# Kernel optimization log

Measured on AMD Instinct MI355X. Metric: run time of the kernel, lower is better.

Reference implementation:

```python
import jax, jax.numpy as jnp
import numpy as np

NUM_HEADS = 12

def get_rel_pos(q_size, k_size, rel_pos):
    # q_size == k_size here; relative index = i - j + (k_size - 1)
    idx = jnp.arange(q_size)[:, None] - jnp.arange(k_size)[None, :] + (k_size - 1)
    return rel_pos[idx]  # (q_size, k_size, head_dim)


def setup_inputs() -> dict:
    key = jax.random.key(0)
    ks = jax.random.split(key, 7)
    B, H, W, C = 1, 64, 64, 768
    return {
        "x": jax.random.normal(ks[0], (B, H, W, C), jnp.float32),
        "w_qkv": jax.random.normal(ks[1], (C, 3 * C), jnp.float32) * 0.02,
        "b_qkv": jnp.zeros((3 * C,), jnp.float32),
        "w_o": jax.random.normal(ks[2], (C, C), jnp.float32) * 0.02,
        "b_o": jnp.zeros((C,), jnp.float32),
        "rel_pos_h": jax.random.normal(ks[3], (2 * H - 1, C // NUM_HEADS), jnp.float32) * 0.02,
        "rel_pos_w": jax.random.normal(ks[4], (2 * W - 1, C // NUM_HEADS), jnp.float32) * 0.02,
    }


def reference(x, w_qkv, b_qkv, w_o, b_o, rel_pos_h, rel_pos_w):
    B, H, W, C = x.shape
    NH = NUM_HEADS
    HD = C // NH
    scale = HD ** -0.5  # 0.125

    qkv = x @ w_qkv + b_qkv                                   # (B,H,W,3C)
    qkv = qkv.reshape(B, H * W, 3, NH, HD)
    qkv = jnp.transpose(qkv, (2, 0, 3, 1, 4)).reshape(3, B * NH, H * W, HD)
    q, k, v = qkv[0], qkv[1], qkv[2]                          # (B*NH, HW, HD)

    Rh = get_rel_pos(H, H, rel_pos_h)                         # (H,H,HD)
    Rw = get_rel_pos(W, W, rel_pos_w)                         # (W,W,HD)
    qr = q.reshape(B * NH, H, W, HD)
    rel_h = jnp.einsum('bhwc,hkc->bhwk', qr, Rh)              # (B*NH,H,W,H)
    rel_w = jnp.einsum('bhwc,wkc->bhwk', qr, Rw)              # (B*NH,H,W,W)

    attn = jnp.einsum('bmd,bnd->bmn', q, k) * scale           # (B*NH,HW,HW)
    attn = attn.reshape(B * NH, H, W, H, W)
    attn = attn + rel_h[:, :, :, :, None] + rel_w[:, :, :, None, :]
    attn = attn.reshape(B * NH, H * W, H * W)

    p = jax.nn.softmax(attn, axis=-1)
    o = jnp.einsum('bmn,bnd->bmd', p, v)                      # (B*NH,HW,HD)
    o = o.reshape(B, NH, H * W, HD)
    o = jnp.transpose(o, (0, 2, 1, 3)).reshape(B, H, W, C)    # heads concat in channel dim
    return o @ w_o + b_o
```

## Files before the change

### kernel.cpp

```cpp
#include <hip/hip_runtime.h>

#define DEVI __device__ __forceinline__
typedef unsigned short u16;
typedef unsigned int u32;
typedef __attribute__((ext_vector_type(4))) float f4v;
typedef __attribute__((ext_vector_type(8))) short bf8v;
typedef __attribute__((ext_vector_type(4))) u32  u32x4;
typedef __attribute__((ext_vector_type(2))) u32  u32x2;
typedef __attribute__((ext_vector_type(4))) u16  u16x4;

#define AS1 __attribute__((address_space(1)))
#define AS3 __attribute__((address_space(3)))

DEVI u16 f2bf(float x){ union{float f;u32 u;} c{x}; u32 r=(c.u+0x7FFFu+((c.u>>16)&1u))>>16; return (u16)r; }
DEVI float bf2f(u16 b){ union{u32 u;float f;} c{(u32)b<<16}; return c.f; }
DEVI f4v mfma32(bf8v a, bf8v b, f4v c){ return __builtin_amdgcn_mfma_f32_16x16x32_bf16(a,b,c,0,0,0); }
DEVI unsigned lds_off(const void* p){ return (unsigned)(unsigned long)(AS3 const void*)p; }
DEVI void glds16(const void* g, void* l){
  __builtin_amdgcn_global_load_lds((AS1 void*)g, (AS3 void*)l, 16, 0, 0);
}

static constexpr int NH = 12, HW = 4096, D = 64, C = 768;
static constexpr float LOG2E = 1.44269504f;

__global__ void qa_convx(const float* __restrict__ x, u16* __restrict__ xb, int n4){
  int i = blockIdx.x*256 + threadIdx.x;
  if(i >= n4) return;
  f4v v = ((const f4v*)x)[i];
  u16x4 o; for(int j=0;j<4;j++) o[j] = f2bf(v[j]);
  ((u16x4*)xb)[i] = o;
}

__global__ void qa_transp(const float* __restrict__ in, u16* __restrict__ out, int R, int Cc){
  __shared__ float tl[32][33];
  int t = threadIdx.x;
  int r0 = blockIdx.y*32, c0 = blockIdx.x*32;
  int tr = t>>3, tc = (t&7)*4;
  f4v v = *(const f4v*)&in[(r0+tr)*Cc + c0 + tc];
  for(int j=0;j<4;j++) tl[tr][tc+j] = v[j];
  __syncthreads();
  int oc = t>>3, orr = (t&7)*4;
  u16x4 o; for(int j=0;j<4;j++) o[j] = f2bf(tl[orr+j][oc]);
  *(u16x4*)&out[(c0+oc)*R + r0 + orr] = o;
}

__global__ __launch_bounds__(256,2) void qa_gemm_qkv(
    const u16* __restrict__ A, const u16* __restrict__ Bt, const float* __restrict__ bias,
    u16* __restrict__ qb, u16* __restrict__ kb, u16* __restrict__ vb){
  __shared__ u16 Al[128*32], Bl[128*32];
  const int t = threadIdx.x, lane = t&63, w = t>>6, c16 = lane&15, h4 = lane>>4;
  const int m0 = blockIdx.y*128, n0 = blockIdx.x*128;
  const int wr = w>>1, wc = w&1;
  f4v acc[4][4] = {};
  for(int k0 = 0; k0 < 768; k0 += 32){
    __syncthreads();
    for(int i=0;i<2;i++){
      int off = i*4096 + w*1024 + lane*16;
      int row = off>>6, kk = (off&63)>>1;
      glds16(A  + (size_t)(m0+row)*768 + k0 + kk, (u16*)Al + i*2048 + w*512);
      glds16(Bt + (size_t)(n0+row)*768 + k0 + kk, (u16*)Bl + i*2048 + w*512);
    }
    __syncthreads();
    bf8v a[4], b[4];
    for(int mt=0;mt<4;mt++) a[mt] = *(const bf8v*)&Al[(wr*64+mt*16+c16)*32 + h4*8];
    for(int nt=0;nt<4;nt++) b[nt] = *(const bf8v*)&Bl[(wc*64+nt*16+c16)*32 + h4*8];
    for(int mt=0;mt<4;mt++) for(int nt=0;nt<4;nt++) acc[mt][nt] = mfma32(a[mt], b[nt], acc[mt][nt]);
  }
  for(int nt=0;nt<4;nt++){
    int col = n0 + wc*64 + nt*16 + c16;
    float bv = bias[col];
    int which = col/768, head = (col>>6)%12, d = col&63;
    u16* dst = which==0 ? qb : (which==1 ? kb : vb);
    float sc = (which==1) ? 0.125f*LOG2E : 1.0f;
    for(int mt=0;mt<4;mt++) for(int r=0;r<4;r++){
      int row = m0 + wr*64 + mt*16 + 4*h4 + r;
      dst[((size_t)(head<<12)+row)*64 + d] = f2bf((acc[mt][nt][r] + bv)*sc);
    }
  }
}

__global__ __launch_bounds__(256) void qa_rel(
    const u16* __restrict__ qbuf, const float* __restrict__ rph, const float* __restrict__ rpw,
    u16* __restrict__ RHt, u16* __restrict__ RW){
  const int t = threadIdx.x, lane = t&63, w = t>>6, c16 = lane&15, h4 = lane>>4;
  const int qh = blockIdx.x, head = blockIdx.y;
  __shared__ u16 ql[64*72], hl[64*72], wl[128*72];
  {
    int row = t>>2, d0 = (t&3)*16;
    const u16* src = qbuf + ((size_t)(head<<12)+(qh<<6)+row)*64 + d0;
    *(u32x4*)&ql[row*72+d0]   = *(const u32x4*)src;
    *(u32x4*)&ql[row*72+d0+8] = *(const u32x4*)(src+8);
    for(int j=0;j<16;j++) hl[row*72+d0+j] = f2bf(rph[(qh+row)*64 + d0 + j]);
    int rw_r = t>>1, rd0 = (t&1)*32;
    for(int j=0;j<32;j++) wl[rw_r*72+rd0+j] = (rw_r<127) ? f2bf(rpw[rw_r*64+rd0+j]) : (u16)0;
  }
  __syncthreads();
  if(w < 2){
    bf8v a[2][2]; f4v acc[2][4] = {};
    for(int mt=0;mt<2;mt++) for(int ch=0;ch<2;ch++)
      a[mt][ch] = *(const bf8v*)&ql[(w*32+mt*16+c16)*72 + ch*32 + h4*8];
    for(int nt=0;nt<4;nt++) for(int ch=0;ch<2;ch++){
      bf8v b = *(const bf8v*)&hl[(nt*16+c16)*72 + ch*32 + h4*8];
      for(int mt=0;mt<2;mt++) acc[mt][nt] = mfma32(a[mt][ch], b, acc[mt][nt]);
    }
    for(int mt=0;mt<2;mt++) for(int nt=0;nt<4;nt++) for(int r=0;r<4;r++){
      int qw = w*32+mt*16+4*h4+r, c = nt*16+c16, kh = 63 - c;
      RHt[((size_t)(head*64+qh)*64+kh)*64 + qw] = f2bf(acc[mt][nt][r]*LOG2E);
    }
  } else {
    bf8v a[2][2]; f4v acc[2][8] = {};
    for(int mt=0;mt<2;mt++) for(int ch=0;ch<2;ch++)
      a[mt][ch] = *(const bf8v*)&ql[((w-2)*32+mt*16+c16)*72 + ch*32 + h4*8];
    for(int nt=0;nt<8;nt++) for(int ch=0;ch<2;ch++){
      bf8v b = *(const bf8v*)&wl[(nt*16+c16)*72 + ch*32 + h4*8];
      for(int mt=0;mt<2;mt++) acc[mt][nt] = mfma32(a[mt][ch], b, acc[mt][nt]);
    }
    for(int mt=0;mt<2;mt++) for(int nt=0;nt<8;nt++) for(int r=0;r<4;r++){
      int qw = (w-2)*32+mt*16+4*h4+r, c = nt*16+c16, kw = qw + 63 - c;
      if((unsigned)kw < 64u) RW[((size_t)(head*64+qh)*64+qw)*64 + kw] = f2bf(acc[mt][nt][r]*LOG2E);
    }
  }
}

__global__ __launch_bounds__(256,3) void qa_attn(
    const u16* __restrict__ qb, const u16* __restrict__ kb, const u16* __restrict__ vb,
    const u16* __restrict__ RHt, const u16* __restrict__ RW, u16* __restrict__ ob){
  __shared__ u16 Kl[2][4096];
  __shared__ u16 Vl[2][4096];
  __shared__ u16 RHl[4096];
  const int t = threadIdx.x, lane = t&63, w = t>>6, c16 = lane&15, h4 = lane>>4;
  const int bid = blockIdx.x;
  const int wid = (bid&7)*96 + (bid>>3);
  const int head = wid>>6, qt = wid&63;

  const u16* rhg = RHt + ((size_t)(head*64+qt))*4096;
  for(int i=0;i<2;i++)
    glds16(rhg + (i*256 + t)*8, (u16*)RHl + (i*256 + w*64)*8);

  int koff[2], voff[2];
  for(int i=0;i<2;i++){
    int u = i*256 + t;
    koff[i] = (u ^ ((u>>3)&7))*8;
    int key = ((u>>1)&3) | (((u>>3)&15)<<2);
    int d0  = ((u&1)<<3) | (((u>>7)&3)<<4);
    voff[i] = key*64 + d0;
  }
  const u16* kg = kb + (size_t)head*262144;
  const u16* vg = vb + (size_t)head*262144;
  const u16* kp = kg; const u16* vp = vg;
  for(int i=0;i<2;i++){
    glds16(kp + koff[i], (u16*)Kl[0] + (i*256 + w*64)*8);
    glds16(vp + voff[i], (u16*)Vl[0] + (i*256 + w*64)*8);
  }
  kp += 4096; vp += 4096;

  const int q0r = qt*64 + w*16;
  bf8v qa[2];
  {
    const u16* qsrc = qb + ((size_t)head*4096 + q0r + c16)*64;
    qa[0] = *(const bf8v*)(qsrc + h4*8);
    qa[1] = *(const bf8v*)(qsrc + 32 + h4*8);
  }
  float rw[4][4];
  for(int nt=0;nt<4;nt++) for(int r=0;r<4;r++){
    int qw = w*16 + c16, kw = nt*16 + 4*h4 + r;
    rw[nt][r] = bf2f(RW[(((size_t)(head*64+qt))*64 + qw)*64 + kw]);
  }

  f4v oacc[4] = {}; float ps = 0.f;
  unsigned vcur = lds_off(Vl) + lane*8;
  const int kq0 = (h4*16) ^ ((c16&7)<<4);
  const int kq1 = (h4*16 + 64) ^ ((c16&7)<<4);
  const int kA  = c16*128;

  for(int kt=0; kt<64; kt++){
    if(kt == 63){ kp = kg; vp = vg; }
    {
      u16* Kn = (u16*)Kl[(kt+1)&1]; u16* Vn = (u16*)Vl[(kt+1)&1];
      for(int i=0;i<2;i++){
        glds16(kp + koff[i], Kn + (i*256 + w*64)*8);
        glds16(vp + voff[i], Vn + (i*256 + w*64)*8);
      }
    }
    kp += 4096; vp += 4096;
    asm volatile("s_waitcnt vmcnt(4)\n\ts_barrier" ::: "memory");

    const char* Kc = (const char*)Kl + (kt&1)*8192;
    float rh = bf2f(RHl[kt*64 + w*16 + c16]);
    f4v p[4];
    #pragma unroll
    for(int nt=0;nt<4;nt++){
      bf8v k0 = *(const bf8v*)(Kc + kA + nt*2048 + kq0);
      bf8v k1 = *(const bf8v*)(Kc + kA + nt*2048 + kq1);
      f4v s;
      for(int r=0;r<4;r++) s[r] = rh + rw[nt][r];
      s = mfma32(k0, qa[0], s);
      s = mfma32(k1, qa[1], s);
      f4v pe;
      for(int r=0;r<4;r++) pe[r] = __builtin_amdgcn_exp2f(s[r]);
      p[nt] = pe;
      ps += pe[0]+pe[1]+pe[2]+pe[3];
    }
    union U8 { u32 w[4]; bf8v v; };
    U8 pb[2];
    #pragma unroll
    for(int half=0;half<2;half++)
      #pragma unroll
      for(int i=0;i<4;i++){
        int nt = half*2 + (i>>1), r0 = (i&1)*2;
        asm("v_cvt_pk_bf16_f32 %0, %1, %2"
            : "=v"(pb[half].w[i]) : "v"(p[nt][r0]), "v"(p[nt][r0+1]));
      }
    #pragma unroll
    for(int dt=0;dt<4;dt++){
      unsigned long t00,t01,t10,t11;
      asm volatile(
        "ds_read_b64_tr_b16 %0, %4 offset:%c5\n\t"
        "ds_read_b64_tr_b16 %1, %4 offset:%c6\n\t"
        "ds_read_b64_tr_b16 %2, %4 offset:%c7\n\t"
        "ds_read_b64_tr_b16 %3, %4 offset:%c8\n\t"
        "s_waitcnt lgkmcnt(0)"
        : "=&v"(t00), "=&v"(t01), "=&v"(t10), "=&v"(t11)
        : "v"(vcur), "i"(dt*2048), "i"(dt*2048+512), "i"(dt*2048+1024), "i"(dt*2048+1536)
        : "memory");
      union { struct{ unsigned long a,b; } q; bf8v v; } v01, v23;
      v01.q.a = t00; v01.q.b = t01; v23.q.a = t10; v23.q.b = t11;
      oacc[dt] = mfma32(v01.v, pb[0].v, oacc[dt]);
      oacc[dt] = mfma32(v23.v, pb[1].v, oacc[dt]);
    }
    asm volatile("s_waitcnt lgkmcnt(0)\n\ts_barrier" ::: "memory");
    vcur ^= 8192;
  }
  asm volatile("s_waitcnt vmcnt(0)" ::: "memory");

  {
    float v = ps;
    v += __shfl_xor(v, 16); v += __shfl_xor(v, 32);
    float inv = 1.0f / v;
    const size_t orow = (size_t)(q0r + c16)*768 + head*64;
    #pragma unroll
    for(int dt=0;dt<4;dt++){
      u16x4 ov;
      for(int r=0;r<4;r++) ov[r] = f2bf(oacc[dt][r]*inv);
      *(u16x4*)&ob[orow + dt*16 + 4*h4] = ov;
    }
  }
}

__global__ __launch_bounds__(256,2) void qa_gemm_out(
    const u16* __restrict__ A, const u16* __restrict__ Bt, const float* __restrict__ bias,
    float* __restrict__ out){
  __shared__ u16 Al[128*32], Bl[128*32];
  const int t = threadIdx.x, lane = t&63, w = t>>6, c16 = lane&15, h4 = lane>>4;
  const int m0 = blockIdx.y*128, n0 = blockIdx.x*128;
  const int wr = w>>1, wc = w&1;
  f4v acc[4][4] = {};
  for(int k0 = 0; k0 < 768; k0 += 32){
    __syncthreads();
    for(int i=0;i<2;i++){
      int off = i*4096 + w*1024 + lane*16;
      int row = off>>6, kk = (off&63)>>1;
      glds16(A  + (size_t)(m0+row)*768 + k0 + kk, (u16*)Al + i*2048 + w*512);
      glds16(Bt + (size_t)(n0+row)*768 + k0 + kk, (u16*)Bl + i*2048 + w*512);
    }
    __syncthreads();
    bf8v a[4], b[4];
    for(int mt=0;mt<4;mt++) a[mt] = *(const bf8v*)&Al[(wr*64+mt*16+c16)*32 + h4*8];
    for(int nt=0;nt<4;nt++) b[nt] = *(const bf8v*)&Bl[(wc*64+nt*16+c16)*32 + h4*8];
    for(int mt=0;mt<4;mt++) for(int nt=0;nt<4;nt++) acc[mt][nt] = mfma32(a[mt], b[nt], acc[mt][nt]);
  }
  for(int nt=0;nt<4;nt++){
    int col = n0 + wc*64 + nt*16 + c16;
    float bv = bias[col];
    for(int mt=0;mt<4;mt++) for(int r=0;r<4;r++){
      int row = m0 + wr*64 + mt*16 + 4*h4 + r;
      out[(size_t)row*768 + col] = acc[mt][nt][r] + bv;
    }
  }
}

extern "C" void kernel_launch(void* const* d_in, const int* in_sizes, int n_in,
                              void* d_out, int out_size, void* d_ws, size_t ws_size,
                              hipStream_t stream){
  const float* x    = (const float*)d_in[0];
  const float* wqkv = (const float*)d_in[1];
  const float* bqkv = (const float*)d_in[2];
  const float* wo   = (const float*)d_in[3];
  const float* bo   = (const float*)d_in[4];
  const float* rph  = (const float*)d_in[5];
  const float* rpw  = (const float*)d_in[6];
  float* out = (float*)d_out;

  size_t off = 0;
  auto alloc = [&](size_t bytes){ void* p = (char*)d_ws + off; off += (bytes + 255) & ~(size_t)255; return p; };
  u16* x_bf   = (u16*)alloc((size_t)HW*C*2);
  u16* wqkv_t = (u16*)alloc((size_t)2304*768*2);
  u16* wo_t   = (u16*)alloc((size_t)768*768*2);
  u16* q_buf  = (u16*)alloc((size_t)NH*HW*D*2);
  u16* k_buf  = (u16*)alloc((size_t)NH*HW*D*2);
  u16* v_buf  = (u16*)alloc((size_t)NH*HW*D*2);
  u16* rh_buf = (u16*)alloc((size_t)NH*64*64*64*2);
  u16* rw_buf = (u16*)alloc((size_t)NH*64*64*64*2);
  u16* o_buf  = (u16*)alloc((size_t)HW*C*2);

  int n4 = HW*C/4;
  qa_convx<<<(n4+255)/256, 256, 0, stream>>>(x, x_bf, n4);
  qa_transp<<<dim3(2304/32, 768/32), 256, 0, stream>>>(wqkv, wqkv_t, 768, 2304);
  qa_transp<<<dim3(768/32, 768/32),  256, 0, stream>>>(wo,   wo_t,   768, 768);
  qa_gemm_qkv<<<dim3(2304/128, HW/128), 256, 0, stream>>>(x_bf, wqkv_t, bqkv, q_buf, k_buf, v_buf);
  qa_rel<<<dim3(64, NH), 256, 0, stream>>>(q_buf, rph, rpw, rh_buf, rw_buf);
  qa_attn<<<768, 256, 0, stream>>>(q_buf, k_buf, v_buf, rh_buf, rw_buf, o_buf);
  qa_gemm_out<<<dim3(768/128, HW/128), 256, 0, stream>>>(o_buf, wo_t, bo, out);
}
```

Baseline: 144.6 us.

## Split attention keys across two blocks with reduce kernel; vectorize GEMM epilogues

Splits each attention query tile's key range across two blocks, doubling the grid, and adds a reduce kernel that sums partial outputs and denominators. GEMMs now preload bias into accumulators, swap MFMA operands for contiguous packed stores, and the K scale is folded into the transposed weights. Also raises attention occupancy bound and adds MFMA priority hints. Adds an extra kernel and bf16 partial-output rounding.

Result: slower. 154.9 us (+7.2%).

```diff
diff --git a/kernel.cpp b/kernel.cpp
--- a/kernel.cpp
+++ b/kernel.cpp
@@ -31,7 +31,7 @@
   ((u16x4*)xb)[i] = o;
 }
 
-__global__ void qa_transp(const float* __restrict__ in, u16* __restrict__ out, int R, int Cc){
+__global__ void qa_transp(const float* __restrict__ in, u16* __restrict__ out, int R, int Cc, int scale_k){
   __shared__ float tl[32][33];
   int t = threadIdx.x;
   int r0 = blockIdx.y*32, c0 = blockIdx.x*32;
@@ -40,7 +40,8 @@
   for(int j=0;j<4;j++) tl[tr][tc+j] = v[j];
   __syncthreads();
   int oc = t>>3, orr = (t&7)*4;
-  u16x4 o; for(int j=0;j<4;j++) o[j] = f2bf(tl[orr+j][oc]);
+  float sc = (scale_k && (c0+oc) >= 768 && (c0+oc) < 1536) ? 0.125f*LOG2E : 1.0f;
+  u16x4 o; for(int j=0;j<4;j++) o[j] = f2bf(tl[orr+j][oc]*sc);
   *(u16x4*)&out[(c0+oc)*R + r0 + orr] = o;
 }
 
@@ -51,7 +52,16 @@
   const int t = threadIdx.x, lane = t&63, w = t>>6, c16 = lane&15, h4 = lane>>4;
   const int m0 = blockIdx.y*128, n0 = blockIdx.x*128;
   const int wr = w>>1, wc = w&1;
-  f4v acc[4][4] = {};
+  f4v acc[4][4];
+  for(int nt=0;nt<4;nt++){
+    f4v bv;
+    for(int r=0;r<4;r++){
+      int col = n0 + wc*64 + nt*16 + 4*h4 + r;
+      float b = bias[col];
+      bv[r] = (col >= 768 && col < 1536) ? b*0.125f*LOG2E : b;
+    }
+    for(int mt=0;mt<4;mt++) acc[mt][nt] = bv;
+  }
   for(int k0 = 0; k0 < 768; k0 += 32){
     __syncthreads();
     for(int i=0;i<2;i++){
@@ -64,17 +74,18 @@
     bf8v a[4], b[4];
     for(int mt=0;mt<4;mt++) a[mt] = *(const bf8v*)&Al[(wr*64+mt*16+c16)*32 + h4*8];
     for(int nt=0;nt<4;nt++) b[nt] = *(const bf8v*)&Bl[(wc*64+nt*16+c16)*32 + h4*8];
-    for(int mt=0;mt<4;mt++) for(int nt=0;nt<4;nt++) acc[mt][nt] = mfma32(a[mt], b[nt], acc[mt][nt]);
-  }
-  for(int nt=0;nt<4;nt++){
-    int col = n0 + wc*64 + nt*16 + c16;
-    float bv = bias[col];
-    int which = col/768, head = (col>>6)%12, d = col&63;
-    u16* dst = which==0 ? qb : (which==1 ? kb : vb);
-    float sc = (which==1) ? 0.125f*LOG2E : 1.0f;
-    for(int mt=0;mt<4;mt++) for(int r=0;r<4;r++){
-      int row = m0 + wr*64 + mt*16 + 4*h4 + r;
-      dst[((size_t)(head<<12)+row)*64 + d] = f2bf((acc[mt][nt][r] + bv)*sc);
+    for(int mt=0;mt<4;mt++) for(int nt=0;nt<4;nt++) acc[mt][nt] = mfma32(b[nt], a[mt], acc[mt][nt]);
+  }
+  for(int mt=0;mt<4;mt++){
+    int row = m0 + wr*64 + mt*16 + c16;
+    for(int nt=0;nt<4;nt++){
+      int col0 = n0 + wc*64 + nt*16 + 4*h4;
+      int which = col0/768, head = (col0>>6)%12, d0 = col0&63;
+      u16* dst = which==0 ? qb : (which==1 ? kb : vb);
+      u32x2 pk;
+      asm("v_cvt_pk_bf16_f32 %0, %1, %2" : "=v"(pk[0]) : "v"(acc[mt][nt][0]), "v"(acc[mt][nt][1]));
+      asm("v_cvt_pk_bf16_f32 %0, %1, %2" : "=v"(pk[1]) : "v"(acc[mt][nt][2]), "v"(acc[mt][nt][3]));
+      *(u32x2*)&dst[((size_t)(head<<12)+row)*64 + d0] = pk;
     }
   }
 }
@@ -122,20 +133,21 @@
   }
 }
 
-__global__ __launch_bounds__(256,3) void qa_attn(
+__global__ __launch_bounds__(256,4) void qa_attn(
     const u16* __restrict__ qb, const u16* __restrict__ kb, const u16* __restrict__ vb,
-    const u16* __restrict__ RHt, const u16* __restrict__ RW, u16* __restrict__ ob){
+    const u16* __restrict__ RHt, const u16* __restrict__ RW,
+    u16* __restrict__ Op, float* __restrict__ Ps){
   __shared__ u16 Kl[2][4096];
   __shared__ u16 Vl[2][4096];
-  __shared__ u16 RHl[4096];
+  __shared__ u16 RHl[2048];
   const int t = threadIdx.x, lane = t&63, w = t>>6, c16 = lane&15, h4 = lane>>4;
   const int bid = blockIdx.x;
-  const int wid = (bid&7)*96 + (bid>>3);
-  const int head = wid>>6, qt = wid&63;
-
-  const u16* rhg = RHt + ((size_t)(head*64+qt))*4096;
-  for(int i=0;i<2;i++)
-    glds16(rhg + (i*256 + t)*8, (u16*)RHl + (i*256 + w*64)*8);
+  const int g = (bid&7)*192 + (bid>>3);
+  const int s = g&1, unit = g>>1;
+  const int head = unit>>6, qt = unit&63;
+
+  const u16* rhg = RHt + (size_t)unit*4096 + s*2048;
+  glds16(rhg + t*8, (u16*)RHl + w*512);
 
   int koff[2], voff[2];
   for(int i=0;i<2;i++){
@@ -145,8 +157,8 @@
     int d0  = ((u&1)<<3) | (((u>>7)&3)<<4);
     voff[i] = key*64 + d0;
   }
-  const u16* kg = kb + (size_t)head*262144;
-  const u16* vg = vb + (size_t)head*262144;
+  const u16* kg = kb + (size_t)head*262144 + (size_t)s*32*4096;
+  const u16* vg = vb + (size_t)head*262144 + (size_t)s*32*4096;
   const u16* kp = kg; const u16* vp = vg;
   for(int i=0;i<2;i++){
     glds16(kp + koff[i], (u16*)Kl[0] + (i*256 + w*64)*8);
@@ -164,19 +176,19 @@
   float rw[4][4];
   for(int nt=0;nt<4;nt++) for(int r=0;r<4;r++){
     int qw = w*16 + c16, kw = nt*16 + 4*h4 + r;
-    rw[nt][r] = bf2f(RW[(((size_t)(head*64+qt))*64 + qw)*64 + kw]);
-  }
-
-  f4v oacc[4] = {}; float ps = 0.f;
+    rw[nt][r] = bf2f(RW[((size_t)unit*64 + qw)*64 + kw]);
+  }
+
+  f4v oacc[4] = {}; f4v psv = {0.f,0.f,0.f,0.f};
   unsigned vcur = lds_off(Vl) + lane*8;
   const int kq0 = (h4*16) ^ ((c16&7)<<4);
   const int kq1 = (h4*16 + 64) ^ ((c16&7)<<4);
   const int kA  = c16*128;
 
-  for(int kt=0; kt<64; kt++){
-    if(kt == 63){ kp = kg; vp = vg; }
+  for(int it=0; it<32; it++){
+    if(it == 31){ kp = kg; vp = vg; }
     {
-      u16* Kn = (u16*)Kl[(kt+1)&1]; u16* Vn = (u16*)Vl[(kt+1)&1];
+      u16* Kn = (u16*)Kl[(it+1)&1]; u16* Vn = (u16*)Vl[(it+1)&1];
       for(int i=0;i<2;i++){
         glds16(kp + koff[i], Kn + (i*256 + w*64)*8);
         glds16(vp + voff[i], Vn + (i*256 + w*64)*8);
@@ -185,21 +197,23 @@
     kp += 4096; vp += 4096;
     asm volatile("s_waitcnt vmcnt(4)\n\ts_barrier" ::: "memory");
 
-    const char* Kc = (const char*)Kl + (kt&1)*8192;
-    float rh = bf2f(RHl[kt*64 + w*16 + c16]);
+    const char* Kc = (const char*)Kl + (it&1)*8192;
+    float rh = bf2f(RHl[it*64 + w*16 + c16]);
     f4v p[4];
     #pragma unroll
     for(int nt=0;nt<4;nt++){
       bf8v k0 = *(const bf8v*)(Kc + kA + nt*2048 + kq0);
       bf8v k1 = *(const bf8v*)(Kc + kA + nt*2048 + kq1);
-      f4v s;
-      for(int r=0;r<4;r++) s[r] = rh + rw[nt][r];
-      s = mfma32(k0, qa[0], s);
-      s = mfma32(k1, qa[1], s);
+      f4v sv;
+      for(int r=0;r<4;r++) sv[r] = rh + rw[nt][r];
+      __builtin_amdgcn_s_setprio(1);
+      sv = mfma32(k0, qa[0], sv);
+      sv = mfma32(k1, qa[1], sv);
+      __builtin_amdgcn_s_setprio(0);
       f4v pe;
-      for(int r=0;r<4;r++) pe[r] = __builtin_amdgcn_exp2f(s[r]);
+      for(int r=0;r<4;r++) pe[r] = __builtin_amdgcn_exp2f(sv[r]);
       p[nt] = pe;
-      ps += pe[0]+pe[1]+pe[2]+pe[3];
+      psv += pe;
     }
     union U8 { u32 w[4]; bf8v v; };
     U8 pb[2];
@@ -225,8 +239,10 @@
         : "memory");
       union { struct{ unsigned long a,b; } q; bf8v v; } v01, v23;
       v01.q.a = t00; v01.q.b = t01; v23.q.a = t10; v23.q.b = t11;
+      __builtin_amdgcn_s_setprio(1);
       oacc[dt] = mfma32(v01.v, pb[0].v, oacc[dt]);
       oacc[dt] = mfma32(v23.v, pb[1].v, oacc[dt]);
+      __builtin_amdgcn_s_setprio(0);
     }
     asm volatile("s_waitcnt lgkmcnt(0)\n\ts_barrier" ::: "memory");
     vcur ^= 8192;
@@ -234,16 +250,35 @@
   asm volatile("s_waitcnt vmcnt(0)" ::: "memory");
 
   {
-    float v = ps;
+    float v = psv[0]+psv[1]+psv[2]+psv[3];
     v += __shfl_xor(v, 16); v += __shfl_xor(v, 32);
-    float inv = 1.0f / v;
-    const size_t orow = (size_t)(q0r + c16)*768 + head*64;
+    const int qrow_l = w*16 + c16;
+    if(h4 == 0) Ps[((size_t)unit*2 + s)*64 + qrow_l] = v;
+    const size_t obase = (((size_t)unit*2 + s)*64 + qrow_l)*64;
     #pragma unroll
     for(int dt=0;dt<4;dt++){
-      u16x4 ov;
-      for(int r=0;r<4;r++) ov[r] = f2bf(oacc[dt][r]*inv);
-      *(u16x4*)&ob[orow + dt*16 + 4*h4] = ov;
-    }
+      u32x2 pk;
+      asm("v_cvt_pk_bf16_f32 %0, %1, %2" : "=v"(pk[0]) : "v"(oacc[dt][0]), "v"(oacc[dt][1]));
+      asm("v_cvt_pk_bf16_f32 %0, %1, %2" : "=v"(pk[1]) : "v"(oacc[dt][2]), "v"(oacc[dt][3]));
+      *(u32x2*)&Op[obase + dt*16 + 4*h4] = pk;
+    }
+  }
+}
+
+__global__ __launch_bounds__(256) void qa_reduce(
+    const u16* __restrict__ Op, const float* __restrict__ Ps, u16* __restrict__ ob){
+  const int unit = blockIdx.x, t = threadIdx.x;
+  const int head = unit>>6, qt = unit&63;
+  const int d0 = (t&15)*4;
+  #pragma unroll
+  for(int qq=0;qq<4;qq++){
+    int qr = (t>>4) + qq*16;
+    float inv = 1.0f / (Ps[((size_t)unit*2)*64 + qr] + Ps[((size_t)unit*2+1)*64 + qr]);
+    u16x4 a = *(const u16x4*)&Op[(((size_t)unit*2  )*64 + qr)*64 + d0];
+    u16x4 b = *(const u16x4*)&Op[(((size_t)unit*2+1)*64 + qr)*64 + d0];
+    u16x4 o;
+    for(int j=0;j<4;j++) o[j] = f2bf((bf2f(a[j]) + bf2f(b[j]))*inv);
+    *(u16x4*)&ob[(size_t)(qt*64 + qr)*768 + head*64 + d0] = o;
   }
 }
 
@@ -254,7 +289,11 @@
   const int t = threadIdx.x, lane = t&63, w = t>>6, c16 = lane&15, h4 = lane>>4;
   const int m0 = blockIdx.y*128, n0 = blockIdx.x*128;
   const int wr = w>>1, wc = w&1;
-  f4v acc[4][4] = {};
+  f4v acc[4][4];
+  for(int nt=0;nt<4;nt++){
+    f4v bv = *(const f4v*)&bias[n0 + wc*64 + nt*16 + 4*h4];
+    for(int mt=0;mt<4;mt++) acc[mt][nt] = bv;
+  }
   for(int k0 = 0; k0 < 768; k0 += 32){
     __syncthreads();
     for(int i=0;i<2;i++){
@@ -267,14 +306,13 @@
     bf8v a[4], b[4];
     for(int mt=0;mt<4;mt++) a[mt] = *(const bf8v*)&Al[(wr*64+mt*16+c16)*32 + h4*8];
     for(int nt=0;nt<4;nt++) b[nt] = *(const bf8v*)&Bl[(wc*64+nt*16+c16)*32 + h4*8];
-    for(int mt=0;mt<4;mt++) for(int nt=0;nt<4;nt++) acc[mt][nt] = mfma32(a[mt], b[nt], acc[mt][nt]);
-  }
-  for(int nt=0;nt<4;nt++){
-    int col = n0 + wc*64 + nt*16 + c16;
-    float bv = bias[col];
-    for(int mt=0;mt<4;mt++) for(int r=0;r<4;r++){
-      int row = m0 + wr*64 + mt*16 + 4*h4 + r;
-      out[(size_t)row*768 + col] = acc[mt][nt][r] + bv;
+    for(int mt=0;mt<4;mt++) for(int nt=0;nt<4;nt++) acc[mt][nt] = mfma32(b[nt], a[mt], acc[mt][nt]);
+  }
+  for(int mt=0;mt<4;mt++){
+    int row = m0 + wr*64 + mt*16 + c16;
+    for(int nt=0;nt<4;nt++){
+      int col0 = n0 + wc*64 + nt*16 + 4*h4;
+      *(f4v*)&out[(size_t)row*768 + col0] = acc[mt][nt];
     }
   }
 }
@@ -302,13 +340,16 @@
   u16* rh_buf = (u16*)alloc((size_t)NH*64*64*64*2);
   u16* rw_buf = (u16*)alloc((size_t)NH*64*64*64*2);
   u16* o_buf  = (u16*)alloc((size_t)HW*C*2);
+  u16* op_buf = (u16*)alloc((size_t)768*2*64*64*2);
+  float* ps_buf = (float*)alloc((size_t)768*2*64*4);
 
   int n4 = HW*C/4;
   qa_convx<<<(n4+255)/256, 256, 0, stream>>>(x, x_bf, n4);
-  qa_transp<<<dim3(2304/32, 768/32), 256, 0, stream>>>(wqkv, wqkv_t, 768, 2304);
-  qa_transp<<<dim3(768/32, 768/32),  256, 0, stream>>>(wo,   wo_t,   768, 768);
+  qa_transp<<<dim3(2304/32, 768/32), 256, 0, stream>>>(wqkv, wqkv_t, 768, 2304, 1);
+  qa_transp<<<dim3(768/32, 768/32),  256, 0, stream>>>(wo,   wo_t,   768, 768, 0);
   qa_gemm_qkv<<<dim3(2304/128, HW/128), 256, 0, stream>>>(x_bf, wqkv_t, bqkv, q_buf, k_buf, v_buf);
   qa_rel<<<dim3(64, NH), 256, 0, stream>>>(q_buf, rph, rpw, rh_buf, rw_buf);
-  qa_attn<<<768, 256, 0, stream>>>(q_buf, k_buf, v_buf, rh_buf, rw_buf, o_buf);
+  qa_attn<<<1536, 256, 0, stream>>>(q_buf, k_buf, v_buf, rh_buf, rw_buf, op_buf, ps_buf);
+  qa_reduce<<<768, 256, 0, stream>>>(op_buf, ps_buf, o_buf);
   qa_gemm_out<<<dim3(768/128, HW/128), 256, 0, stream>>>(o_buf, wo_t, bo, out);
 }
```
